# Optimization experiments

Measured on AMD Instinct MI355X. Metric: run time of the kernel, lower is better.

## Reference

```python
import jax, jax.numpy as jnp
import numpy as np

B, N, D = 8, 256, 128


def setup_inputs() -> dict:
    key = jax.random.key(0)
    ks = jax.random.split(key, 4)
    s1 = 1.0 / np.sqrt(4 * D)
    s2 = 1.0 / np.sqrt(2 * D)
    s3 = 1.0 / np.sqrt(D)
    return {
        "tour_features": jax.random.normal(ks[0], (B, N, D), dtype=jnp.float32),
        "W1": jax.random.uniform(ks[1], (4 * D, 2 * D), jnp.float32, -s1, s1),
        "b1": jnp.zeros((2 * D,), jnp.float32),
        "W2": jax.random.uniform(ks[2], (2 * D, D), jnp.float32, -s2, s2),
        "b2": jnp.zeros((D,), jnp.float32),
        "W3": jax.random.uniform(ks[3], (D, 1), jnp.float32, -s3, s3),
        "b3": jnp.zeros((1,), jnp.float32),
    }


def reference(tour_features, W1, b1, W2, b2, W3, b3):
    Bs, Ns, Ds = tour_features.shape
    x = tour_features
    x_next = jnp.roll(x, -1, axis=1)  # node at (k+1) % N
    # Split first linear's weight by the 4 concatenated feature blocks:
    # cat([x_i, x_{i+1}, x_j, x_{j+1}]) @ W1 == x_i@W1a + x_{i+1}@W1b + x_j@W1c + x_{j+1}@W1d
    W1a, W1b, W1c, W1d = jnp.split(W1, 4, axis=0)
    Pi = x @ W1a + x_next @ W1b          # [B, N, 2D] (i-side projection)
    Pj = x @ W1c + x_next @ W1d          # [B, N, 2D] (j-side projection)
    h1 = jax.nn.relu(Pi[:, :, None, :] + Pj[:, None, :, :] + b1)  # [B, N, N, 2D]
    h2 = jax.nn.relu(h1 @ W2 + b2)       # [B, N, N, D]
    score = jnp.tanh((h2 @ W3 + b3)[..., 0])  # [B, N, N]
    # Valid pairs: j >= i + 2 and not (j - i == N - 1)
    ii = jnp.arange(Ns)[:, None]
    jj = jnp.arange(Ns)[None, :]
    mask = (jj >= ii + 2) & (jj - ii != Ns - 1)
    improvement_matrix = jnp.where(mask[None], score, 0.0)
    improved_tour = jnp.broadcast_to(jnp.arange(Ns), (Bs, Ns))
    return improved_tour, improvement_matrix
```

## Files before the change

### kernel.cpp

```cpp
#include <hip/hip_runtime.h>


typedef __attribute__((ext_vector_type(8))) short short8;
typedef __attribute__((ext_vector_type(8))) _Float16 half8;
typedef __attribute__((ext_vector_type(4))) float floatx4;

static __device__ __forceinline__ unsigned short f2bf(float f) {
  unsigned int x = __float_as_uint(f);
  x += 0x7fff + ((x >> 16) & 1);
  return (unsigned short)(x >> 16);
}

static __device__ __forceinline__ unsigned short f2h(float f) {
  _Float16 h = (_Float16)f;
  return __builtin_bit_cast(unsigned short, h);
}

static __device__ __forceinline__ float fast_tanh(float x) {
  float e = __expf(2.0f * fabsf(x));
  float t = 1.0f - 2.0f * __builtin_amdgcn_rcpf(e + 1.0f);
  return copysignf(t, x);
}

__global__ __launch_bounds__(256) void k_prep(
    const float* __restrict__ x, const float* __restrict__ W1,
    const float* __restrict__ W2, float* __restrict__ out,
    unsigned short* __restrict__ W2H, unsigned short* __restrict__ W1T,
    unsigned short* __restrict__ xcat) {
  int e = blockIdx.x * 256 + threadIdx.x;
  if (e < 2048) {
    out[e] = (float)(e & 255);
  } else if (e < 34816) {
    int e2 = e - 2048;
    int k = e2 >> 7, n = e2 & 127;
    W2H[n * 256 + k] = f2h(W2[e2]);
  } else if (e < 165888) {
    int e3 = e - 34816;
    int n = e3 >> 8, k = e3 & 255;
    W1T[e3] = f2bf(W1[((k + (n & 256)) << 8) + (n & 255)]);
  } else {
    int e4 = e - 165888;
    int r = e4 >> 8, k = e4 & 255;
    int pos = r & 255;
    int pos2 = (k < 128) ? pos : ((pos + 1) & 255);
    xcat[e4] = f2bf(x[(((r >> 8) << 8) + pos2) * 128 + (k & 127)]);
  }
}

__global__ __launch_bounds__(256) void k_proj(
    const unsigned short* __restrict__ xcat, const unsigned short* __restrict__ W1T,
    const float* __restrict__ b1, unsigned short* __restrict__ PiH,
    unsigned short* __restrict__ PjH) {
  const int mg = blockIdx.x >> 3;
  const int ng = blockIdx.x & 7;
  const int tid = threadIdx.x;
  const int wr = tid >> 6, lane = tid & 63, quad = lane >> 4, l15 = lane & 15;

  __shared__ unsigned short As[64 * 256];
  __shared__ unsigned short Bs[64 * 256];

#pragma unroll
  for (int it = 0; it < 8; ++it) {
    int e = it * 256 + tid;
    int r = e >> 5, v = e & 31;
    int col = ((v & 16) | ((v ^ (r & 15)) & 15)) << 3;
    *(uint4*)&As[r * 256 + col] = *(const uint4*)(xcat + (mg * 64 + r) * 256 + v * 8);
    *(uint4*)&Bs[r * 256 + col] = *(const uint4*)(W1T + (ng * 64 + r) * 256 + v * 8);
  }
  __syncthreads();

  floatx4 acc[4];
#pragma unroll
  for (int mt = 0; mt < 4; ++mt) acc[mt] = (floatx4)0.f;

  const char* Ab = (const char*)As;
  const char* Bb = (const char*)Bs + wr * 16 * 512;
  const int base_sw = l15 * 512 + ((quad ^ l15) << 4);

#pragma unroll
  for (int ks = 0; ks < 8; ++ks) {
    const int swz = base_sw ^ (ks << 6);
    short8 bfr = *(const short8*)(Bb + swz);
#pragma unroll
    for (int mt = 0; mt < 4; ++mt) {
      short8 afr = *(const short8*)(Ab + mt * 8192 + swz);
      acc[mt] = __builtin_amdgcn_mfma_f32_16x16x32_bf16(afr, bfr, acc[mt], 0, 0, 0);
    }
  }

  const int ch = ng * 64 + wr * 16 + l15;
  const float bias = (ch < 256) ? b1[ch] : 0.f;
  unsigned short* dst = (ch < 256) ? PiH : PjH;
  const int chan = ch & 255;
#pragma unroll
  for (int mt = 0; mt < 4; ++mt)
#pragma unroll
    for (int r = 0; r < 4; ++r) {
      int row = mg * 64 + mt * 16 + quad * 4 + r;
      dst[row * 256 + chan] = f2h(acc[mt][r] + bias);
    }
}

__global__ __launch_bounds__(512, 4) void k_main(
    const unsigned short* __restrict__ PiH, const unsigned short* __restrict__ PjH,
    const unsigned short* __restrict__ W2H, const float* __restrict__ b2,
    const float* __restrict__ W3, const float* __restrict__ b3,
    float* __restrict__ outm) {
  const int bid = blockIdx.x;
  const int b = bid >> 7;
  const int ig = bid & 127;
  const int tid = threadIdx.x;
  const int wr = tid >> 6;
  const int lane = tid & 63, quad = lane >> 4, l15 = lane & 15;

  __shared__ unsigned short W2s[128][256];

#pragma unroll
  for (int it = 0; it < 8; ++it) {
    int e = it * 512 + tid;
    int n = e >> 5, v = e & 31;
    int col = ((v & 16) | ((v ^ (n & 15)) & 15)) << 3;
    *(uint4*)&W2s[n][col] = *(const uint4*)(W2H + n * 256 + v * 8);
  }
  __syncthreads();

  const char* W2base = (const char*)&W2s[0][0];
  const int base_sw = l15 * 512 + ((quad ^ l15) << 4);
  const unsigned short* Pjb = PjH + ((b << 8) + wr * 32 + l15) * 256 + quad * 8;

#pragma unroll
  for (int ii = 0; ii < 2; ++ii) {
    const int i = ii ? (255 - ig) : ig;
    float* orow = outm + ((b << 8) + i) * 256 + wr * 32;
    if (i > wr * 32 + 29) {
      if (lane < 32) orow[lane] = 0.f;
      continue;
    }

    floatx4 acc[2][8];
#pragma unroll
    for (int mt = 0; mt < 2; ++mt)
#pragma unroll
      for (int nt = 0; nt < 8; ++nt) acc[mt][nt] = (floatx4)0.f;

    const unsigned short* PiRow = PiH + ((b << 8) + i) * 256 + quad * 8;

    union U4 { uint4 v; half8 h; };
    U4 piR[2], pjR[2][2];
    piR[0].v = *(const uint4*)(PiRow);
    pjR[0][0].v = *(const uint4*)(Pjb);
    pjR[0][1].v = *(const uint4*)(Pjb + 4096);

#pragma unroll
    for (int ks = 0; ks < 8; ++ks) {
      const int cur = ks & 1, nxt = cur ^ 1;
      if (ks < 7) {
        piR[nxt].v = *(const uint4*)(PiRow + (ks + 1) * 32);
        pjR[nxt][0].v = *(const uint4*)(Pjb + (ks + 1) * 32);
        pjR[nxt][1].v = *(const uint4*)(Pjb + 4096 + (ks + 1) * 32);
      }
      const half8 af0 = __builtin_elementwise_max(piR[cur].h + pjR[cur][0].h,
                                                  (half8)(_Float16)0);
      const half8 af1 = __builtin_elementwise_max(piR[cur].h + pjR[cur][1].h,
                                                  (half8)(_Float16)0);
      const char* baddr = W2base + (base_sw ^ (ks << 6));
#pragma unroll
      for (int nt = 0; nt < 8; ++nt) {
        half8 bfr = *(const half8*)(baddr + nt * 8192);
        acc[0][nt] = __builtin_amdgcn_mfma_f32_16x16x32_f16(af0, bfr, acc[0][nt], 0, 0, 0);
        acc[1][nt] = __builtin_amdgcn_mfma_f32_16x16x32_f16(af1, bfr, acc[1][nt], 0, 0, 0);
      }
    }

    const float b3v = b3[0];
#pragma unroll
    for (int mt = 0; mt < 2; ++mt) {
      float p0 = 0, p1 = 0, p2 = 0, p3 = 0;
#pragma unroll
      for (int nt = 0; nt < 8; ++nt) {
        float w3v = W3[nt * 16 + l15];
        float b2v = b2[nt * 16 + l15];
        floatx4 a = acc[mt][nt];
        p0 += fmaxf(a[0] + b2v, 0.f) * w3v;
        p1 += fmaxf(a[1] + b2v, 0.f) * w3v;
        p2 += fmaxf(a[2] + b2v, 0.f) * w3v;
        p3 += fmaxf(a[3] + b2v, 0.f) * w3v;
      }
#pragma unroll
      for (int m = 8; m >= 1; m >>= 1) {
        p0 += __shfl_xor(p0, m, 16);
        p1 += __shfl_xor(p1, m, 16);
        p2 += __shfl_xor(p2, m, 16);
        p3 += __shfl_xor(p3, m, 16);
      }
      if (l15 == 0) {
        const int jl = wr * 32 + mt * 16 + quad * 4;
        float ps[4] = {p0, p1, p2, p3};
#pragma unroll
        for (int r = 0; r < 4; ++r) {
          int j = jl + r;
          float s = fast_tanh(ps[r] + b3v);
          bool valid = (j >= i + 2) && (j - i != 255);
          orow[mt * 16 + quad * 4 + r] = valid ? s : 0.f;
        }
      }
    }
  }
}

extern "C" void kernel_launch(void* const* d_in, const int* in_sizes, int n_in,
                              void* d_out, int out_size, void* d_ws, size_t ws_size,
                              hipStream_t stream) {
  const float* x  = (const float*)d_in[0];
  const float* W1 = (const float*)d_in[1];
  const float* b1 = (const float*)d_in[2];
  const float* W2 = (const float*)d_in[3];
  const float* b2 = (const float*)d_in[4];
  const float* W3 = (const float*)d_in[5];
  const float* b3 = (const float*)d_in[6];
  float* out = (float*)d_out;

  unsigned short* PiH  = (unsigned short*)d_ws;
  unsigned short* PjH  = PiH + 524288;
  unsigned short* W2H  = PjH + 524288;
  unsigned short* W1T  = W2H + 32768;
  unsigned short* xcat = W1T + 131072;

  k_prep<<<2696, 256, 0, stream>>>(x, W1, W2, out, W2H, W1T, xcat);
  k_proj<<<256, 256, 0, stream>>>(xcat, W1T, b1, PiH, PjH);
  k_main<<<1024, 512, 0, stream>>>(PiH, PjH, W2H, b2, W3, b3, out + 2048);
}
```

Baseline: 110.7 us.

## Remap main kernel to enumerate only valid triangular (i, j-tile) work items

The main kernel previously launched blocks over every (i, wave j-tile) pair and skipped invalid lower-triangle tiles, which left waves idle and produced load imbalance. Now each wave is given a unique (j-tile, i) item taken from a packed triangular enumeration across a 142x8 grid, so only tiles with valid pairs are computed. The zeroing of the output matrix moves into the prep kernel, which writes the whole matrix before the main kernel overwrites the valid tiles. This costs an extra full-matrix write in prep and a fixed W2 LDS load per block that now serves fewer useful waves.

```diff
diff --git a/kernel.cpp b/kernel.cpp
--- a/kernel.cpp
+++ b/kernel.cpp
@@ -30,16 +30,18 @@
   int e = blockIdx.x * 256 + threadIdx.x;
   if (e < 2048) {
     out[e] = (float)(e & 255);
-  } else if (e < 34816) {
-    int e2 = e - 2048;
+  } else if (e < 526336) {
+    out[e] = 0.f;
+  } else if (e < 559104) {
+    int e2 = e - 526336;
     int k = e2 >> 7, n = e2 & 127;
     W2H[n * 256 + k] = f2h(W2[e2]);
-  } else if (e < 165888) {
-    int e3 = e - 34816;
+  } else if (e < 690176) {
+    int e3 = e - 559104;
     int n = e3 >> 8, k = e3 & 255;
     W1T[e3] = f2bf(W1[((k + (n & 256)) << 8) + (n & 255)]);
   } else {
-    int e4 = e - 165888;
+    int e4 = e - 690176;
     int r = e4 >> 8, k = e4 & 255;
     int pos = r & 255;
     int pos2 = (k < 128) ? pos : ((pos + 1) & 255);
@@ -106,9 +108,7 @@
     const unsigned short* __restrict__ W2H, const float* __restrict__ b2,
     const float* __restrict__ W3, const float* __restrict__ b3,
     float* __restrict__ outm) {
-  const int bid = blockIdx.x;
-  const int b = bid >> 7;
-  const int ig = bid & 127;
+  const int b = blockIdx.y;
   const int tid = threadIdx.x;
   const int wr = tid >> 6;
   const int lane = tid & 63, quad = lane >> 4, l15 = lane & 15;
@@ -124,85 +124,86 @@
   }
   __syncthreads();
 
+  const int e = blockIdx.x * 8 + wr;
+  int jt = 0, base = 0;
+  if (e >= 30)  { jt = 1; base = 30;  }
+  if (e >= 92)  { jt = 2; base = 92;  }
+  if (e >= 186) { jt = 3; base = 186; }
+  if (e >= 312) { jt = 4; base = 312; }
+  if (e >= 470) { jt = 5; base = 470; }
+  if (e >= 660) { jt = 6; base = 660; }
+  if (e >= 882) { jt = 7; base = 882; }
+  const int i = e - base;
+
   const char* W2base = (const char*)&W2s[0][0];
   const int base_sw = l15 * 512 + ((quad ^ l15) << 4);
-  const unsigned short* Pjb = PjH + ((b << 8) + wr * 32 + l15) * 256 + quad * 8;
-
-#pragma unroll
-  for (int ii = 0; ii < 2; ++ii) {
-    const int i = ii ? (255 - ig) : ig;
-    float* orow = outm + ((b << 8) + i) * 256 + wr * 32;
-    if (i > wr * 32 + 29) {
-      if (lane < 32) orow[lane] = 0.f;
-      continue;
-    }
-
-    floatx4 acc[2][8];
-#pragma unroll
-    for (int mt = 0; mt < 2; ++mt)
-#pragma unroll
-      for (int nt = 0; nt < 8; ++nt) acc[mt][nt] = (floatx4)0.f;
-
-    const unsigned short* PiRow = PiH + ((b << 8) + i) * 256 + quad * 8;
-
-    union U4 { uint4 v; half8 h; };
-    U4 piR[2], pjR[2][2];
-    piR[0].v = *(const uint4*)(PiRow);
-    pjR[0][0].v = *(const uint4*)(Pjb);
-    pjR[0][1].v = *(const uint4*)(Pjb + 4096);
-
-#pragma unroll
-    for (int ks = 0; ks < 8; ++ks) {
-      const int cur = ks & 1, nxt = cur ^ 1;
-      if (ks < 7) {
-        piR[nxt].v = *(const uint4*)(PiRow + (ks + 1) * 32);
-        pjR[nxt][0].v = *(const uint4*)(Pjb + (ks + 1) * 32);
-        pjR[nxt][1].v = *(const uint4*)(Pjb + 4096 + (ks + 1) * 32);
-      }
-      const half8 af0 = __builtin_elementwise_max(piR[cur].h + pjR[cur][0].h,
-                                                  (half8)(_Float16)0);
-      const half8 af1 = __builtin_elementwise_max(piR[cur].h + pjR[cur][1].h,
-                                                  (half8)(_Float16)0);
-      const char* baddr = W2base + (base_sw ^ (ks << 6));
-#pragma unroll
-      for (int nt = 0; nt < 8; ++nt) {
-        half8 bfr = *(const half8*)(baddr + nt * 8192);
-        acc[0][nt] = __builtin_amdgcn_mfma_f32_16x16x32_f16(af0, bfr, acc[0][nt], 0, 0, 0);
-        acc[1][nt] = __builtin_amdgcn_mfma_f32_16x16x32_f16(af1, bfr, acc[1][nt], 0, 0, 0);
-      }
-    }
-
-    const float b3v = b3[0];
-#pragma unroll
-    for (int mt = 0; mt < 2; ++mt) {
-      float p0 = 0, p1 = 0, p2 = 0, p3 = 0;
-#pragma unroll
-      for (int nt = 0; nt < 8; ++nt) {
-        float w3v = W3[nt * 16 + l15];
-        float b2v = b2[nt * 16 + l15];
-        floatx4 a = acc[mt][nt];
-        p0 += fmaxf(a[0] + b2v, 0.f) * w3v;
-        p1 += fmaxf(a[1] + b2v, 0.f) * w3v;
-        p2 += fmaxf(a[2] + b2v, 0.f) * w3v;
-        p3 += fmaxf(a[3] + b2v, 0.f) * w3v;
-      }
-#pragma unroll
-      for (int m = 8; m >= 1; m >>= 1) {
-        p0 += __shfl_xor(p0, m, 16);
-        p1 += __shfl_xor(p1, m, 16);
-        p2 += __shfl_xor(p2, m, 16);
-        p3 += __shfl_xor(p3, m, 16);
-      }
-      if (l15 == 0) {
-        const int jl = wr * 32 + mt * 16 + quad * 4;
-        float ps[4] = {p0, p1, p2, p3};
-#pragma unroll
-        for (int r = 0; r < 4; ++r) {
-          int j = jl + r;
-          float s = fast_tanh(ps[r] + b3v);
-          bool valid = (j >= i + 2) && (j - i != 255);
-          orow[mt * 16 + quad * 4 + r] = valid ? s : 0.f;
-        }
+  const unsigned short* Pjb = PjH + ((b << 8) + jt * 32 + l15) * 256 + quad * 8;
+  const unsigned short* PiRow = PiH + ((b << 8) + i) * 256 + quad * 8;
+
+  floatx4 acc[2][8];
+#pragma unroll
+  for (int mt = 0; mt < 2; ++mt)
+#pragma unroll
+    for (int nt = 0; nt < 8; ++nt) acc[mt][nt] = (floatx4)0.f;
+
+  union U4 { uint4 v; half8 h; };
+  U4 piR[2], pjR[2][2];
+  piR[0].v = *(const uint4*)(PiRow);
+  pjR[0][0].v = *(const uint4*)(Pjb);
+  pjR[0][1].v = *(const uint4*)(Pjb + 4096);
+
+#pragma unroll
+  for (int ks = 0; ks < 8; ++ks) {
+    const int cur = ks & 1, nxt = cur ^ 1;
+    if (ks < 7) {
+      piR[nxt].v = *(const uint4*)(PiRow + (ks + 1) * 32);
+      pjR[nxt][0].v = *(const uint4*)(Pjb + (ks + 1) * 32);
+      pjR[nxt][1].v = *(const uint4*)(Pjb + 4096 + (ks + 1) * 32);
+    }
+    const half8 af0 = __builtin_elementwise_max(piR[cur].h + pjR[cur][0].h,
+                                                (half8)(_Float16)0);
+    const half8 af1 = __builtin_elementwise_max(piR[cur].h + pjR[cur][1].h,
+                                                (half8)(_Float16)0);
+    const char* baddr = W2base + (base_sw ^ (ks << 6));
+#pragma unroll
+    for (int nt = 0; nt < 8; ++nt) {
+      half8 bfr = *(const half8*)(baddr + nt * 8192);
+      acc[0][nt] = __builtin_amdgcn_mfma_f32_16x16x32_f16(af0, bfr, acc[0][nt], 0, 0, 0);
+      acc[1][nt] = __builtin_amdgcn_mfma_f32_16x16x32_f16(af1, bfr, acc[1][nt], 0, 0, 0);
+    }
+  }
+
+  float* orow = outm + ((b << 8) + i) * 256 + jt * 32;
+  const float b3v = b3[0];
+#pragma unroll
+  for (int mt = 0; mt < 2; ++mt) {
+    float p0 = 0, p1 = 0, p2 = 0, p3 = 0;
+#pragma unroll
+    for (int nt = 0; nt < 8; ++nt) {
+      float w3v = W3[nt * 16 + l15];
+      float b2v = b2[nt * 16 + l15];
+      floatx4 a = acc[mt][nt];
+      p0 += fmaxf(a[0] + b2v, 0.f) * w3v;
+      p1 += fmaxf(a[1] + b2v, 0.f) * w3v;
+      p2 += fmaxf(a[2] + b2v, 0.f) * w3v;
+      p3 += fmaxf(a[3] + b2v, 0.f) * w3v;
+    }
+#pragma unroll
+    for (int m = 8; m >= 1; m >>= 1) {
+      p0 += __shfl_xor(p0, m, 16);
+      p1 += __shfl_xor(p1, m, 16);
+      p2 += __shfl_xor(p2, m, 16);
+      p3 += __shfl_xor(p3, m, 16);
+    }
+    if (l15 == 0) {
+      const int jl = jt * 32 + mt * 16 + quad * 4;
+      float ps[4] = {p0, p1, p2, p3};
+#pragma unroll
+      for (int r = 0; r < 4; ++r) {
+        int j = jl + r;
+        float s = fast_tanh(ps[r] + b3v);
+        bool valid = (j >= i + 2) && (j - i != 255);
+        orow[mt * 16 + quad * 4 + r] = valid ? s : 0.f;
       }
     }
   }
@@ -226,7 +227,8 @@
   unsigned short* W1T  = W2H + 32768;
   unsigned short* xcat = W1T + 131072;
 
-  k_prep<<<2696, 256, 0, stream>>>(x, W1, W2, out, W2H, W1T, xcat);
+  k_prep<<<4744, 256, 0, stream>>>(x, W1, W2, out, W2H, W1T, xcat);
   k_proj<<<256, 256, 0, stream>>>(xcat, W1T, b1, PiH, PjH);
-  k_main<<<1024, 512, 0, stream>>>(PiH, PjH, W2H, b2, W3, b3, out + 2048);
-}
+  dim3 grid_main(142, 8);
+  k_main<<<grid_main, 512, 0, stream>>>(PiH, PjH, W2H, b2, W3, b3, out + 2048);
+}
```

After: 105.9 us. 1.05x faster.
